# Performance work log

Measured on AMD Instinct MI355X. Metric: run time of the kernel, lower is better.

The kernel has to match this reference:

```python
import jax, jax.numpy as jnp
import numpy as np

CHF_STEP = 32
CHF_TIK = 0.05
SAMPLE_STEP = 1.0
IS_DENSE = False


def _make_templates(H, W, dtype):
    # sample coordinates of pixel centers; x over width (last dim), y over height
    x_axis = SAMPLE_STEP / 2 + SAMPLE_STEP * jnp.arange(W, dtype=dtype)  # (W,)
    y_axis = SAMPLE_STEP / 2 + SAMPLE_STEP * jnp.arange(H, dtype=dtype)  # (H,)
    # matches torch: repeat_interleave(x, H) and y.repeat(W) -> column-major flatten order
    coords = jnp.stack([jnp.repeat(x_axis, H), jnp.tile(y_axis, W)], axis=0)  # (2, N=W*H)
    freq = jnp.arange(-CHF_STEP, CHF_STEP, dtype=dtype) * CHF_TIK  # (2S,)
    S2 = 2 * CHF_STEP
    # plane[u, v] = (freq[v], freq[u])
    plane = jnp.stack([jnp.broadcast_to(freq[None, :], (S2, S2)),
                       jnp.broadcast_to(freq[:, None], (S2, S2))], axis=2)  # (2S, 2S, 2)
    angle = jnp.einsum('uvc,cn->uvn', plane, coords)  # (2S, 2S, N)
    return jnp.cos(angle), jnp.sin(angle)


def setup_inputs() -> dict:
    key = jax.random.key(0)
    k1, k2 = jax.random.split(key)
    B, H, W = 16, 128, 128
    dnn_output = jax.random.uniform(k1, (B, H, W), dtype=jnp.float32)
    chf = jax.random.normal(k2, (B, 2 * CHF_STEP, 2 * CHF_STEP, 2), dtype=jnp.float32)
    return {"dnn_output": dnn_output, "chf": chf}


def reference(dnn_output, chf):
    B, H, W = dnn_output.shape
    real_t, img_t = _make_templates(H, W, dnn_output.dtype)  # (2S,2S,N) each
    # transpose(-1,-2) then flatten -> column-major order matching coords
    flat = jnp.swapaxes(dnn_output, -1, -2).reshape(B, -1)  # (B, N)
    # broadcast-multiply + sum == batched GEMM
    chf_real = jnp.einsum('uvn,bn->buv', real_t, flat)
    chf_img = jnp.einsum('uvn,bn->buv', img_t, flat)
    derived = jnp.stack([chf_real, chf_img], axis=3).astype(chf.dtype)  # (B,2S,2S,2)
    diff = derived - chf
    if IS_DENSE:
        loss = jnp.sum(jnp.linalg.norm(diff, axis=2)) * (CHF_TIK ** 2)
    else:
        loss = jnp.sum(jnp.linalg.norm(diff.reshape(B, -1), axis=1) * CHF_TIK)
    return loss / B
```

## Files before the change

kernel.cpp:

```cpp
#include <hip/hip_runtime.h>
#include <math.h>

#define S2 64
#define HH 128
#define WW 128
#define BB 16
#define TIK 0.05f
#define NU 33
#define NBLK (BB * NU)

#define ROT(c, s, cr, sr)                    \
    {                                        \
        const float _cn = fmaf(c, cr, -(s) * (sr)); \
        s = fmaf(s, cr, (c) * (sr));         \
        c = _cn;                             \
    }

__global__ __launch_bounds__(256) void chf_main(const float* __restrict__ dnn,
                                                const float* __restrict__ chf,
                                                float* __restrict__ partials) {
    const int bid = blockIdx.x;
    const int b = bid / NU;
    const int uu = bid - b * NU;
    const int t = threadIdx.x;

    __shared__ float a2r[8 * WW], a2i[8 * WW];
    __shared__ float crw[WW], ciw[WW];
    __shared__ float prc[256], prs[256], pic[256], pis[256];

    const float fu = (float)(uu - 32) * TIK;

    float2 cf = make_float2(0.f, 0.f), cfm = make_float2(0.f, 0.f);
    if (t < 64) {
        cf = *(const float2*)(chf + ((((size_t)b * S2 + uu) * S2 + t) * 2));
        if (uu >= 1 && uu <= 31)
            cfm = *(const float2*)(chf + ((((size_t)b * S2 + (64 - uu)) * S2 + t) * 2));
    }

    {
        const int hg = t >> 5;
        const int w4 = (t & 31) << 2;
        const float4* drow = (const float4*)(dnn + (size_t)b * HH * WW);

        const float a0 = fu * ((float)(hg * 16) + 0.5f);
        float c0 = __cosf(a0), s0 = __sinf(a0);
        const float cfu = __cosf(fu), sfu = __sinf(fu);
        float c1 = c0, s1 = s0;
        ROT(c1, s1, cfu, sfu);
        const float c2s = fmaf(cfu, cfu, -sfu * sfu);
        const float s2s = 2.0f * sfu * cfu;

        float ar0 = 0, ar1 = 0, ar2 = 0, ar3 = 0;
        float ai0 = 0, ai1 = 0, ai2 = 0, ai3 = 0;
#pragma unroll
        for (int j = 0; j < 8; ++j) {
            const int h = hg * 16 + 2 * j;
            const float4 d0 = drow[h * (WW / 4) + (w4 >> 2)];
            const float4 d1 = drow[(h + 1) * (WW / 4) + (w4 >> 2)];
            ar0 = fmaf(c0, d0.x, ar0); ai0 = fmaf(s0, d0.x, ai0);
            ar1 = fmaf(c0, d0.y, ar1); ai1 = fmaf(s0, d0.y, ai1);
            ar2 = fmaf(c0, d0.z, ar2); ai2 = fmaf(s0, d0.z, ai2);
            ar3 = fmaf(c0, d0.w, ar3); ai3 = fmaf(s0, d0.w, ai3);
            ar0 = fmaf(c1, d1.x, ar0); ai0 = fmaf(s1, d1.x, ai0);
            ar1 = fmaf(c1, d1.y, ar1); ai1 = fmaf(s1, d1.y, ai1);
            ar2 = fmaf(c1, d1.z, ar2); ai2 = fmaf(s1, d1.z, ai2);
            ar3 = fmaf(c1, d1.w, ar3); ai3 = fmaf(s1, d1.w, ai3);
            ROT(c0, s0, c2s, s2s);
            ROT(c1, s1, c2s, s2s);
        }
        *(float4*)&a2r[hg * WW + w4] = make_float4(ar0, ar1, ar2, ar3);
        *(float4*)&a2i[hg * WW + w4] = make_float4(ai0, ai1, ai2, ai3);
    }
    __syncthreads();

    if (t < WW) {
        float sr = 0, si = 0;
#pragma unroll
        for (int g = 0; g < 8; ++g) {
            sr += a2r[g * WW + t];
            si += a2i[g * WW + t];
        }
        crw[t] = sr;
        ciw[t] = si;
    }
    __syncthreads();

    {
        const int v = t & 63;
        const int q = t >> 6;
        const int w0 = q * 32;
        const float fv = (float)(v - 32) * TIK;

        const float a0 = fv * ((float)w0 + 0.5f);
        float c0 = __cosf(a0), s0 = __sinf(a0);
        const float cfv = __cosf(fv), sfv = __sinf(fv);
        float c1 = c0, s1 = s0; ROT(c1, s1, cfv, sfv);
        float c2 = c1, s2 = s1; ROT(c2, s2, cfv, sfv);
        float c3 = c2, s3 = s2; ROT(c3, s3, cfv, sfv);
        const float c2f = fmaf(cfv, cfv, -sfv * sfv);
        const float s2f = 2.0f * sfv * cfv;
        const float c4f = fmaf(c2f, c2f, -s2f * s2f);
        const float s4f = 2.0f * s2f * c2f;

        float rc = 0, rs = 0, ic = 0, is_ = 0;
#pragma unroll
        for (int j = 0; j < 8; ++j) {
            const int w = w0 + 4 * j;
            float cr, ci;
            cr = crw[w];     ci = ciw[w];
            rc = fmaf(c0, cr, rc); rs = fmaf(s0, cr, rs);
            ic = fmaf(c0, ci, ic); is_ = fmaf(s0, ci, is_);
            cr = crw[w + 1]; ci = ciw[w + 1];
            rc = fmaf(c1, cr, rc); rs = fmaf(s1, cr, rs);
            ic = fmaf(c1, ci, ic); is_ = fmaf(s1, ci, is_);
            cr = crw[w + 2]; ci = ciw[w + 2];
            rc = fmaf(c2, cr, rc); rs = fmaf(s2, cr, rs);
            ic = fmaf(c2, ci, ic); is_ = fmaf(s2, ci, is_);
            cr = crw[w + 3]; ci = ciw[w + 3];
            rc = fmaf(c3, cr, rc); rs = fmaf(s3, cr, rs);
            ic = fmaf(c3, ci, ic); is_ = fmaf(s3, ci, is_);
            ROT(c0, s0, c4f, s4f);
            ROT(c1, s1, c4f, s4f);
            ROT(c2, s2, c4f, s4f);
            ROT(c3, s3, c4f, s4f);
        }
        prc[t] = rc; prs[t] = rs; pic[t] = ic; pis[t] = is_;
    }
    __syncthreads();

    if (t < 64) {
        const float rc = prc[t] + prc[t + 64] + prc[t + 128] + prc[t + 192];
        const float rs = prs[t] + prs[t + 64] + prs[t + 128] + prs[t + 192];
        const float ic = pic[t] + pic[t + 64] + pic[t + 128] + pic[t + 192];
        const float is_ = pis[t] + pis[t + 64] + pis[t + 128] + pis[t + 192];

        const float d0 = (rc - is_) - cf.x;
        const float d1 = (rs + ic) - cf.y;
        float sq = fmaf(d0, d0, d1 * d1);

        if (uu >= 1 && uu <= 31) {
            const float d2 = (rc + is_) - cfm.x;
            const float d3 = (rs - ic) - cfm.y;
            sq = fmaf(d2, d2, sq);
            sq = fmaf(d3, d3, sq);
        }
#pragma unroll
        for (int off = 32; off; off >>= 1)
            sq += __shfl_down(sq, off, 64);
        if (t == 0) partials[bid] = sq;
    }
}

__global__ __launch_bounds__(1024) void chf_final(const float* __restrict__ partials,
                                                  float* __restrict__ out) {
    const int t = threadIdx.x;
    const int b = t >> 6;
    const int l = t & 63;
    __shared__ float red[BB];
    float v = (l < NU) ? partials[b * NU + l] : 0.0f;
#pragma unroll
    for (int off = 32; off; off >>= 1)
        v += __shfl_down(v, off, 64);
    if (l == 0) red[b] = sqrtf(v);
    __syncthreads();
    if (t == 0) {
        float acc = 0;
#pragma unroll
        for (int i = 0; i < BB; ++i) acc += red[i];
        out[0] = acc * (TIK / (float)BB);
    }
}

extern "C" void kernel_launch(void* const* d_in, const int* in_sizes, int n_in,
                              void* d_out, int out_size, void* d_ws, size_t ws_size,
                              hipStream_t stream) {
    const float* dnn = (const float*)d_in[0];
    const float* chf = (const float*)d_in[1];
    float* out = (float*)d_out;
    float* partials = (float*)d_ws;

    chf_main<<<dim3(NBLK), dim3(256), 0, stream>>>(dnn, chf, partials);
    chf_final<<<dim3(1), dim3(1024), 0, stream>>>(partials, out);
}
```

Measured before the change: 11.47 us.

## Process two u-frequency rows per block to reuse dnn loads and v-twiddles

Each block now computes two u rows (uu=2g and 2g+1) instead of one, halving the grid from 528 to 272 blocks. The dnn tile loads in the first stage and the v-direction twiddles in the second stage are shared across both rows. The final reduction kernel shrinks to 512 threads with 32-lane groups to match. The trade-off is more registers and roughly double the shared memory per block, fewer blocks to fill the GPU, and a last group that does a single row and wastes half its work.

```diff
diff --git a/kernel.cpp b/kernel.cpp
--- a/kernel.cpp
+++ b/kernel.cpp
@@ -6,82 +6,110 @@
 #define WW 128
 #define BB 16
 #define TIK 0.05f
-#define NU 33
-#define NBLK (BB * NU)
-
-#define ROT(c, s, cr, sr)                    \
-    {                                        \
+#define NG 17
+#define NBLK (BB * NG)
+
+#define ROT(c, s, cr, sr)                           \
+    {                                               \
         const float _cn = fmaf(c, cr, -(s) * (sr)); \
-        s = fmaf(s, cr, (c) * (sr));         \
-        c = _cn;                             \
-    }
+        s = fmaf(s, cr, (c) * (sr));                \
+        c = _cn;                                    \
+    }
+
+#define FMA4(acc, sc, v)                \
+    acc.x = fmaf(sc, v.x, acc.x);       \
+    acc.y = fmaf(sc, v.y, acc.y);       \
+    acc.z = fmaf(sc, v.z, acc.z);       \
+    acc.w = fmaf(sc, v.w, acc.w);
 
 __global__ __launch_bounds__(256) void chf_main(const float* __restrict__ dnn,
                                                 const float* __restrict__ chf,
                                                 float* __restrict__ partials) {
     const int bid = blockIdx.x;
-    const int b = bid / NU;
-    const int uu = bid - b * NU;
+    const int b = bid / NG;
+    const int g = bid - b * NG;
     const int t = threadIdx.x;
-
-    __shared__ float a2r[8 * WW], a2i[8 * WW];
-    __shared__ float crw[WW], ciw[WW];
-    __shared__ float prc[256], prs[256], pic[256], pis[256];
-
-    const float fu = (float)(uu - 32) * TIK;
-
-    float2 cf = make_float2(0.f, 0.f), cfm = make_float2(0.f, 0.f);
+    const bool dual = (g < 16);
+    const int uu0 = dual ? (g << 1) : 32;
+    const int uu1 = (g << 1) + 1;
+
+    __shared__ float a2r0[8 * WW], a2i0[8 * WW], a2r1[8 * WW], a2i1[8 * WW];
+    __shared__ float crw0[WW], ciw0[WW], crw1[WW], ciw1[WW];
+    __shared__ float prc0[256], prs0[256], pic0[256], pis0[256];
+    __shared__ float prc1[256], prs1[256], pic1[256], pis1[256];
+
+    const float fu0 = (float)(uu0 - 32) * TIK;
+    const float fu1 = (float)(uu1 - 32) * TIK;
+
+    float2 cf0 = make_float2(0.f, 0.f), cfm0 = make_float2(0.f, 0.f);
+    float2 cf1 = make_float2(0.f, 0.f), cfm1 = make_float2(0.f, 0.f);
     if (t < 64) {
-        cf = *(const float2*)(chf + ((((size_t)b * S2 + uu) * S2 + t) * 2));
-        if (uu >= 1 && uu <= 31)
-            cfm = *(const float2*)(chf + ((((size_t)b * S2 + (64 - uu)) * S2 + t) * 2));
+        cf0 = *(const float2*)(chf + ((((size_t)b * S2 + uu0) * S2 + t) * 2));
+        if (uu0 >= 1 && uu0 <= 31)
+            cfm0 = *(const float2*)(chf + ((((size_t)b * S2 + (64 - uu0)) * S2 + t) * 2));
+        if (dual) {
+            cf1 = *(const float2*)(chf + ((((size_t)b * S2 + uu1) * S2 + t) * 2));
+            cfm1 = *(const float2*)(chf + ((((size_t)b * S2 + (64 - uu1)) * S2 + t) * 2));
+        }
     }
 
     {
         const int hg = t >> 5;
-        const int w4 = (t & 31) << 2;
+        const int w4 = t & 31;
         const float4* drow = (const float4*)(dnn + (size_t)b * HH * WW);
 
-        const float a0 = fu * ((float)(hg * 16) + 0.5f);
-        float c0 = __cosf(a0), s0 = __sinf(a0);
-        const float cfu = __cosf(fu), sfu = __sinf(fu);
-        float c1 = c0, s1 = s0;
-        ROT(c1, s1, cfu, sfu);
-        const float c2s = fmaf(cfu, cfu, -sfu * sfu);
-        const float s2s = 2.0f * sfu * cfu;
-
-        float ar0 = 0, ar1 = 0, ar2 = 0, ar3 = 0;
-        float ai0 = 0, ai1 = 0, ai2 = 0, ai3 = 0;
+        const float base = (float)(hg * 16) + 0.5f;
+        float c00 = __cosf(fu0 * base), s00 = __sinf(fu0 * base);
+        const float cA = __cosf(fu0), sA = __sinf(fu0);
+        float c01 = c00, s01 = s00;
+        ROT(c01, s01, cA, sA);
+        const float c2A = fmaf(cA, cA, -sA * sA), s2A = 2.0f * sA * cA;
+
+        float c10 = 0.f, s10 = 0.f, c11 = 0.f, s11 = 0.f;
+        float c2B = 1.f, s2B = 0.f;
+        if (dual) {
+            c10 = __cosf(fu1 * base); s10 = __sinf(fu1 * base);
+            const float cB = __cosf(fu1), sB = __sinf(fu1);
+            c11 = c10; s11 = s10;
+            ROT(c11, s11, cB, sB);
+            c2B = fmaf(cB, cB, -sB * sB); s2B = 2.0f * sB * cB;
+        }
+
+        float4 ar0 = {0, 0, 0, 0}, ai0 = {0, 0, 0, 0};
+        float4 ar1 = {0, 0, 0, 0}, ai1 = {0, 0, 0, 0};
 #pragma unroll
         for (int j = 0; j < 8; ++j) {
             const int h = hg * 16 + 2 * j;
-            const float4 d0 = drow[h * (WW / 4) + (w4 >> 2)];
-            const float4 d1 = drow[(h + 1) * (WW / 4) + (w4 >> 2)];
-            ar0 = fmaf(c0, d0.x, ar0); ai0 = fmaf(s0, d0.x, ai0);
-            ar1 = fmaf(c0, d0.y, ar1); ai1 = fmaf(s0, d0.y, ai1);
-            ar2 = fmaf(c0, d0.z, ar2); ai2 = fmaf(s0, d0.z, ai2);
-            ar3 = fmaf(c0, d0.w, ar3); ai3 = fmaf(s0, d0.w, ai3);
-            ar0 = fmaf(c1, d1.x, ar0); ai0 = fmaf(s1, d1.x, ai0);
-            ar1 = fmaf(c1, d1.y, ar1); ai1 = fmaf(s1, d1.y, ai1);
-            ar2 = fmaf(c1, d1.z, ar2); ai2 = fmaf(s1, d1.z, ai2);
-            ar3 = fmaf(c1, d1.w, ar3); ai3 = fmaf(s1, d1.w, ai3);
-            ROT(c0, s0, c2s, s2s);
-            ROT(c1, s1, c2s, s2s);
-        }
-        *(float4*)&a2r[hg * WW + w4] = make_float4(ar0, ar1, ar2, ar3);
-        *(float4*)&a2i[hg * WW + w4] = make_float4(ai0, ai1, ai2, ai3);
+            const float4 d0 = drow[h * (WW / 4) + w4];
+            const float4 d1 = drow[(h + 1) * (WW / 4) + w4];
+            FMA4(ar0, c00, d0); FMA4(ai0, s00, d0);
+            FMA4(ar0, c01, d1); FMA4(ai0, s01, d1);
+            FMA4(ar1, c10, d0); FMA4(ai1, s10, d0);
+            FMA4(ar1, c11, d1); FMA4(ai1, s11, d1);
+            ROT(c00, s00, c2A, s2A);
+            ROT(c01, s01, c2A, s2A);
+            ROT(c10, s10, c2B, s2B);
+            ROT(c11, s11, c2B, s2B);
+        }
+        const int idx = hg * WW + w4 * 4;
+        *(float4*)&a2r0[idx] = ar0;
+        *(float4*)&a2i0[idx] = ai0;
+        *(float4*)&a2r1[idx] = ar1;
+        *(float4*)&a2i1[idx] = ai1;
     }
     __syncthreads();
 
     if (t < WW) {
-        float sr = 0, si = 0;
-#pragma unroll
-        for (int g = 0; g < 8; ++g) {
-            sr += a2r[g * WW + t];
-            si += a2i[g * WW + t];
-        }
-        crw[t] = sr;
-        ciw[t] = si;
+        float sr0 = 0, si0 = 0, sr1 = 0, si1 = 0;
+#pragma unroll
+        for (int k = 0; k < 8; ++k) {
+            sr0 += a2r0[k * WW + t];
+            si0 += a2i0[k * WW + t];
+            sr1 += a2r1[k * WW + t];
+            si1 += a2i1[k * WW + t];
+        }
+        crw0[t] = sr0; ciw0[t] = si0;
+        crw1[t] = sr1; ciw1[t] = si1;
     }
     __syncthreads();
 
@@ -102,47 +130,65 @@
         const float c4f = fmaf(c2f, c2f, -s2f * s2f);
         const float s4f = 2.0f * s2f * c2f;
 
-        float rc = 0, rs = 0, ic = 0, is_ = 0;
+        float rc0 = 0, rs0 = 0, ic0 = 0, is0 = 0;
+        float rc1 = 0, rs1 = 0, ic1 = 0, is1 = 0;
+#define BSTEP(CK, SK, W)                                          \
+        {                                                         \
+            const float cr0v = crw0[W], ci0v = ciw0[W];           \
+            const float cr1v = crw1[W], ci1v = ciw1[W];           \
+            rc0 = fmaf(CK, cr0v, rc0); rs0 = fmaf(SK, cr0v, rs0); \
+            ic0 = fmaf(CK, ci0v, ic0); is0 = fmaf(SK, ci0v, is0); \
+            rc1 = fmaf(CK, cr1v, rc1); rs1 = fmaf(SK, cr1v, rs1); \
+            ic1 = fmaf(CK, ci1v, ic1); is1 = fmaf(SK, ci1v, is1); \
+        }
 #pragma unroll
         for (int j = 0; j < 8; ++j) {
             const int w = w0 + 4 * j;
-            float cr, ci;
-            cr = crw[w];     ci = ciw[w];
-            rc = fmaf(c0, cr, rc); rs = fmaf(s0, cr, rs);
-            ic = fmaf(c0, ci, ic); is_ = fmaf(s0, ci, is_);
-            cr = crw[w + 1]; ci = ciw[w + 1];
-            rc = fmaf(c1, cr, rc); rs = fmaf(s1, cr, rs);
-            ic = fmaf(c1, ci, ic); is_ = fmaf(s1, ci, is_);
-            cr = crw[w + 2]; ci = ciw[w + 2];
-            rc = fmaf(c2, cr, rc); rs = fmaf(s2, cr, rs);
-            ic = fmaf(c2, ci, ic); is_ = fmaf(s2, ci, is_);
-            cr = crw[w + 3]; ci = ciw[w + 3];
-            rc = fmaf(c3, cr, rc); rs = fmaf(s3, cr, rs);
-            ic = fmaf(c3, ci, ic); is_ = fmaf(s3, ci, is_);
+            BSTEP(c0, s0, w);
+            BSTEP(c1, s1, w + 1);
+            BSTEP(c2, s2, w + 2);
+            BSTEP(c3, s3, w + 3);
             ROT(c0, s0, c4f, s4f);
             ROT(c1, s1, c4f, s4f);
             ROT(c2, s2, c4f, s4f);
             ROT(c3, s3, c4f, s4f);
         }
-        prc[t] = rc; prs[t] = rs; pic[t] = ic; pis[t] = is_;
+#undef BSTEP
+        prc0[t] = rc0; prs0[t] = rs0; pic0[t] = ic0; pis0[t] = is0;
+        prc1[t] = rc1; prs1[t] = rs1; pic1[t] = ic1; pis1[t] = is1;
     }
     __syncthreads();
 
     if (t < 64) {
-        const float rc = prc[t] + prc[t + 64] + prc[t + 128] + prc[t + 192];
-        const float rs = prs[t] + prs[t + 64] + prs[t + 128] + prs[t + 192];
-        const float ic = pic[t] + pic[t + 64] + pic[t + 128] + pic[t + 192];
-        const float is_ = pis[t] + pis[t + 64] + pis[t + 128] + pis[t + 192];
-
-        const float d0 = (rc - is_) - cf.x;
-        const float d1 = (rs + ic) - cf.y;
+        const float rc = prc0[t] + prc0[t + 64] + prc0[t + 128] + prc0[t + 192];
+        const float rs = prs0[t] + prs0[t + 64] + prs0[t + 128] + prs0[t + 192];
+        const float ic = pic0[t] + pic0[t + 64] + pic0[t + 128] + pic0[t + 192];
+        const float is_ = pis0[t] + pis0[t + 64] + pis0[t + 128] + pis0[t + 192];
+
+        const float d0 = (rc - is_) - cf0.x;
+        const float d1 = (rs + ic) - cf0.y;
         float sq = fmaf(d0, d0, d1 * d1);
-
-        if (uu >= 1 && uu <= 31) {
-            const float d2 = (rc + is_) - cfm.x;
-            const float d3 = (rs - ic) - cfm.y;
+        if (uu0 >= 1 && uu0 <= 31) {
+            const float d2 = (rc + is_) - cfm0.x;
+            const float d3 = (rs - ic) - cfm0.y;
             sq = fmaf(d2, d2, sq);
             sq = fmaf(d3, d3, sq);
+        }
+
+        if (dual) {
+            const float rcB = prc1[t] + prc1[t + 64] + prc1[t + 128] + prc1[t + 192];
+            const float rsB = prs1[t] + prs1[t + 64] + prs1[t + 128] + prs1[t + 192];
+            const float icB = pic1[t] + pic1[t + 64] + pic1[t + 128] + pic1[t + 192];
+            const float isB = pis1[t] + pis1[t + 64] + pis1[t + 128] + pis1[t + 192];
+
+            const float e0 = (rcB - isB) - cf1.x;
+            const float e1 = (rsB + icB) - cf1.y;
+            sq = fmaf(e0, e0, sq);
+            sq = fmaf(e1, e1, sq);
+            const float e2 = (rcB + isB) - cfm1.x;
+            const float e3 = (rsB - icB) - cfm1.y;
+            sq = fmaf(e2, e2, sq);
+            sq = fmaf(e3, e3, sq);
         }
 #pragma unroll
         for (int off = 32; off; off >>= 1)
@@ -151,16 +197,16 @@
     }
 }
 
-__global__ __launch_bounds__(1024) void chf_final(const float* __restrict__ partials,
-                                                  float* __restrict__ out) {
+__global__ __launch_bounds__(512) void chf_final(const float* __restrict__ partials,
+                                                 float* __restrict__ out) {
     const int t = threadIdx.x;
-    const int b = t >> 6;
-    const int l = t & 63;
+    const int b = t >> 5;
+    const int l = t & 31;
     __shared__ float red[BB];
-    float v = (l < NU) ? partials[b * NU + l] : 0.0f;
-#pragma unroll
-    for (int off = 32; off; off >>= 1)
-        v += __shfl_down(v, off, 64);
+    float v = (l < NG) ? partials[b * NG + l] : 0.0f;
+#pragma unroll
+    for (int off = 16; off; off >>= 1)
+        v += __shfl_down(v, off, 32);
     if (l == 0) red[b] = sqrtf(v);
     __syncthreads();
     if (t == 0) {
@@ -180,5 +226,5 @@
     float* partials = (float*)d_ws;
 
     chf_main<<<dim3(NBLK), dim3(256), 0, stream>>>(dnn, chf, partials);
-    chf_final<<<dim3(1), dim3(1024), 0, stream>>>(partials, out);
+    chf_final<<<dim3(1), dim3(512), 0, stream>>>(partials, out);
 }
```

Measured after the change: 11.75 us. +2.4%, slower.
